# Kernel optimization log

Hardware: AMD Instinct MI355X
Metric: run time of the kernel (lower is better)

Reference implementation:

```python
import jax, jax.numpy as jnp
import numpy as np

B, N, C, F = 8, 3, 64, 128
H = W = 128


def _up2(x):
    # nearest-neighbor upsample by 2 on the last two axes
    return jnp.repeat(jnp.repeat(x, 2, axis=-2), 2, axis=-1)


def setup_inputs() -> dict:
    key = jax.random.key(0)
    ks = jax.random.split(key, 12)
    s = lambda k, shp, fan: jax.random.normal(k, shp, jnp.float32) * (1.0 / np.sqrt(fan))
    return {
        "contexts": jax.random.normal(ks[0], (B, N, C, H, W), jnp.float32),
        "mainstream": jax.random.normal(ks[1], (B, F, H // 2, W // 2), jnp.float32),
        "Wc": s(ks[2], (C, C), C),        # W_context 1x1 conv weight [out,in]
        "bc": jnp.zeros((C,), jnp.float32),
        "Wf": s(ks[3], (C, F), F),        # W_feat 1x1
        "bf": jnp.zeros((C,), jnp.float32),
        "Wk": s(ks[4], (C, F), F),        # W_key_feat 1x1
        "bk": jnp.zeros((C,), jnp.float32),
        "Vw": s(ks[5], (C, F, 3, 3), F * 9),  # values_conv 3x3, OIHW
        "Vb": jnp.zeros((C,), jnp.float32),
    }


def reference(contexts, mainstream, Wc, bc, Wf, bf, Wk, bk, Vw, Vb):
    # contexts: [B,N,C,H,W], mainstream: [B,F,h,w]
    bias = lambda b: b[None, :, None, None]
    queries = jnp.einsum('bfhw,cf->bchw', mainstream, Wf) + bias(bf)       # [B,C,h,w]
    keys_m = jnp.einsum('bfhw,cf->bchw', mainstream, Wk) + bias(bk)        # [B,C,h,w]
    values = jax.lax.conv_general_dilated(
        mainstream, Vw, (1, 1), 'SAME',
        dimension_numbers=('NCHW', 'OIHW', 'NCHW')) + bias(Vb)             # [B,C,h,w]

    # stack contexts with upsampled mainstream keys, project with W_context (1x1)
    keys_stack = jnp.concatenate([contexts, _up2(keys_m)[:, None]], axis=1)  # [B,N+1,C,H,W]
    keys_proj = jnp.einsum('bnchw,dc->bndhw', keys_stack, Wc) + bc[None, None, :, None, None]

    q_up = _up2(queries)                                                    # [B,C,H,W]
    logits = jnp.einsum('bnchw,bchw->bnhw', keys_proj, q_up)                # [B,N+1,H,W]
    attn = jax.nn.softmax(logits, axis=1)                                   # softmax over contexts

    vals_stack = jnp.concatenate([contexts, _up2(values)[:, None]], axis=1) # [B,N+1,C,H,W]
    out = jnp.einsum('bnchw,bnhw->bchw', vals_stack, attn)                  # [B,C,H,W]
    return out
```

## Files before the change

kernel.cpp:

```cpp
#include <hip/hip_runtime.h>
#include <math.h>

#define CH   64
#define FD   128
#define HS   64
#define FS   128
#define NB   8
#define NCTX 3

#define WS_BQ   4227072
#define WS_AVH  4227136
#define WS_AQH  4264000
#define WS_AQL  4268096
#define WS_AKH  4272192
#define WS_AKL  4276288

typedef short  s16x8  __attribute__((ext_vector_type(8)));
typedef float  f32x16 __attribute__((ext_vector_type(16)));

__device__ inline unsigned short bf16_rne(float x) {
  unsigned u = __float_as_uint(x);
  u += 0x7FFFu + ((u >> 16) & 1u);
  return (unsigned short)(u >> 16);
}
__device__ inline void split2(float x, unsigned short& h, unsigned short& l) {
  h = bf16_rne(x);
  l = bf16_rne(x - __uint_as_float((unsigned)h << 16));
}

__global__ __launch_bounds__(256) void afrag_prep(
    const float* __restrict__ Wc, const float* __restrict__ Wf,
    const float* __restrict__ bf, const float* __restrict__ Wk,
    const float* __restrict__ Vw, float* __restrict__ ws) {
  int id = blockIdx.x * 256 + threadIdx.x;
  unsigned short* avh = (unsigned short*)(ws + WS_AVH);
  unsigned short* aqh = (unsigned short*)(ws + WS_AQH);
  unsigned short* aql = (unsigned short*)(ws + WS_AQL);
  unsigned short* akh = (unsigned short*)(ws + WS_AKH);
  unsigned short* akl = (unsigned short*)(ws + WS_AKL);

  if (id < 9216) {
    int tile = id / 4608, rem = id % 4608;
    int q = rem >> 6, l = rem & 63;
    int am = l & 31, kh = l >> 5;
    int c = tile * 32 + am, tap = q >> 3, kf = q & 7;
#pragma unroll
    for (int j = 0; j < 8; ++j) {
      int f = kf * 16 + kh * 8 + j;
      avh[id * 8 + j] = bf16_rne(Vw[(c * FD + f) * 9 + tap]);
    }
  } else if (id < 10240) {
    int i2 = id - 9216;
    int tile = i2 >> 9, rem = i2 & 511;
    int q = rem >> 6, l = rem & 63;
    int am = l & 31, kh = l >> 5;
    int c = tile * 32 + am;
#pragma unroll
    for (int j = 0; j < 8; ++j) {
      int f = q * 16 + kh * 8 + j;
      float acc = 0.f;
      for (int d = 0; d < CH; ++d)
        acc = fmaf(Wc[d * CH + c], Wf[d * FD + f], acc);
      unsigned short h, lo; split2(acc, h, lo);
      aqh[i2 * 8 + j] = h; aql[i2 * 8 + j] = lo;
    }
  } else if (id < 11264) {
    int i3 = id - 10240;
    int tile = i3 >> 9, rem = i3 & 511;
    int q = rem >> 6, l = rem & 63;
    int am = l & 31, kh = l >> 5;
    int c = tile * 32 + am;
#pragma unroll
    for (int j = 0; j < 8; ++j) {
      int f = q * 16 + kh * 8 + j;
      unsigned short h, lo; split2(Wk[c * FD + f], h, lo);
      akh[i3 * 8 + j] = h; akl[i3 * 8 + j] = lo;
    }
  } else if (id < 11328) {
    int c = id - 11264;
    float acc = 0.f;
    for (int d = 0; d < CH; ++d) acc = fmaf(Wc[d * CH + c], bf[d], acc);
    ws[WS_BQ + c] = acc;
  }
}

__global__ __launch_bounds__(512) void fused_kernel(
    const float* __restrict__ m, const float* __restrict__ Vb,
    const float* __restrict__ bk, const float* __restrict__ ctx,
    float* __restrict__ out, const float* __restrict__ ws) {
  const int b = blockIdx.x >> 6, y = blockIdx.x & 63;
  const int t = threadIdx.x, lane = t & 63;
  const int wave = __builtin_amdgcn_readfirstlane(t >> 6);
  const int am = lane & 31, kh = lane >> 5;

  __shared__ __align__(16) union {
    short HI[3][8][66][2][8];
    struct {
      float  QT[CH * HS];
      float  VAL[CH * HS];
      float4 wpart[2][4][3][16];
      float  L3row[HS];
    } p;
  } U;
  __shared__ float l3red[2][64];

  if (t < 96) {
    int row = t / 32, kf = (t >> 2) & 7, khh = (t >> 1) & 1, col = (t & 1) * 65;
    s16x8 z;
#pragma unroll
    for (int j = 0; j < 8; ++j) z[j] = 0;
    *(s16x8*)&U.HI[row][kf][col][khh][0] = z;
  }

#pragma unroll
  for (int i = 0; i < 6; ++i) {
    const int tk = wave * 6 + i;
    const int row = tk >> 4, kf = (tk >> 1) & 7, khh = tk & 1;
    const int yy = y + row - 1;
    s16x8 hi;
    if (yy >= 0 && yy < HS) {
#pragma unroll
      for (int j = 0; j < 8; ++j) {
        const int f = kf * 16 + khh * 8 + j;
        hi[j] = (short)bf16_rne(m[((b * FD + f) * HS + yy) * HS + lane]);
      }
    } else {
#pragma unroll
      for (int j = 0; j < 8; ++j) hi[j] = 0;
    }
    *(s16x8*)&U.HI[row][kf][lane + 1][khh][0] = hi;
  }
  __syncthreads();

  const int ct = (wave >> 1) & 1;
  const int xh = wave & 1;
  const int x0 = xh * 32, ch0 = ct * 32;

  f32x16 acc, q1, q2, k1, k2;
  float l3part = 0.f;

  if (wave < 4) {
    const unsigned short* avh = (const unsigned short*)(ws + WS_AVH);
#pragma unroll
    for (int i = 0; i < 16; ++i) acc[i] = 0.f;
#pragma unroll 8
    for (int q = 0; q < 72; ++q) {
      const int tap = q >> 3, kf = q & 7;
      const s16x8 ah = *(const s16x8*)(avh + ((ct * 72 + q) * 64 + lane) * 8);
      const s16x8 bh = *(const s16x8*)&U.HI[tap / 3][kf][x0 + am + tap % 3][kh][0];
      acc = __builtin_amdgcn_mfma_f32_32x32x16_bf16(ah, bh, acc, 0, 0, 0);
    }
  } else {
    const unsigned short* aqh = (const unsigned short*)(ws + WS_AQH);
    const unsigned short* aql = (const unsigned short*)(ws + WS_AQL);
    const unsigned short* akh = (const unsigned short*)(ws + WS_AKH);
    const unsigned short* akl = (const unsigned short*)(ws + WS_AKL);
#pragma unroll
    for (int i = 0; i < 16; ++i) { q1[i] = 0.f; q2[i] = 0.f; k1[i] = 0.f; k2[i] = 0.f; }
#pragma unroll
    for (int q = 0; q < 8; ++q) {
      const s16x8 bh = *(const s16x8*)&U.HI[1][q][x0 + am + 1][kh][0];
      s16x8 bl;
#pragma unroll
      for (int j = 0; j < 8; ++j) {
        const float mv = m[((b * FD + q * 16 + kh * 8 + j) * HS + y) * HS + x0 + am];
        const float hf = __uint_as_float(((unsigned)(unsigned short)bh[j]) << 16);
        bl[j] = (short)bf16_rne(mv - hf);
      }
      const s16x8 ah = *(const s16x8*)(aqh + ((ct * 8 + q) * 64 + lane) * 8);
      const s16x8 al = *(const s16x8*)(aql + ((ct * 8 + q) * 64 + lane) * 8);
      const s16x8 kah = *(const s16x8*)(akh + ((ct * 8 + q) * 64 + lane) * 8);
      const s16x8 kal = *(const s16x8*)(akl + ((ct * 8 + q) * 64 + lane) * 8);
      q1 = __builtin_amdgcn_mfma_f32_32x32x16_bf16(ah, bh, q1, 0, 0, 0);
      q1 = __builtin_amdgcn_mfma_f32_32x32x16_bf16(al, bh, q1, 0, 0, 0);
      q2 = __builtin_amdgcn_mfma_f32_32x32x16_bf16(ah, bl, q2, 0, 0, 0);
      k1 = __builtin_amdgcn_mfma_f32_32x32x16_bf16(kah, bh, k1, 0, 0, 0);
      k1 = __builtin_amdgcn_mfma_f32_32x32x16_bf16(kal, bh, k1, 0, 0, 0);
      k2 = __builtin_amdgcn_mfma_f32_32x32x16_bf16(kah, bl, k2, 0, 0, 0);
    }
  }
  __syncthreads();

  if (wave < 4) {
#pragma unroll
    for (int r = 0; r < 16; ++r) {
      const int c = ch0 + (r & 3) + 8 * (r >> 2) + 4 * kh;
      U.p.VAL[c * HS + x0 + am] = acc[r] + Vb[c];
    }
  } else {
#pragma unroll
    for (int r = 0; r < 16; ++r) {
      const int c = ch0 + (r & 3) + 8 * (r >> 2) + 4 * kh;
      const float qvv = q1[r] + q2[r] + ws[WS_BQ + c];
      const float kvv = k1[r] + k2[r] + bk[c];
      U.p.QT[c * HS + x0 + am] = qvv;
      l3part = fmaf(qvv, kvv, l3part);
    }
    if (ct == 1) l3red[xh][lane] = l3part;
  }
  __syncthreads();

  if (wave == 4 || wave == 5) {
    float s = l3part + l3red[xh][lane];
    s += __shfl_xor(s, 32, 64);
    if (kh == 0) U.p.L3row[x0 + am] = s;
  }
  __syncthreads();

  const int u    = t >> 8;
  const int tt   = t & 255;
  const int quad = tt & 15;
  const int cg   = tt >> 4;
  const int wv   = tt >> 6;
  const int c0   = cg * 4;
  const int hrow = 2 * y + u;
  const int cs = FS * FS, ns = CH * FS * FS;

  float* op = out + (size_t)(b * CH) * FS * FS + (size_t)hrow * FS;
  const float* cb = ctx + (size_t)(b * NCTX * CH) * cs + (size_t)hrow * FS;

#pragma unroll 1
  for (int x2 = 0; x2 < 2; ++x2) {
    const int x = x2 * 64 + quad * 4;
    const int w2 = x >> 1;

    float4 cv[3][4];
    float2 qv[4];
#pragma unroll
    for (int j = 0; j < 4; ++j) {
      const int c = c0 + j;
      cv[0][j] = *(const float4*)(cb + x + c * cs);
      cv[1][j] = *(const float4*)(cb + x + ns + c * cs);
      cv[2][j] = *(const float4*)(cb + x + 2 * ns + c * cs);
      qv[j] = *(const float2*)&U.p.QT[c * HS + w2];
    }

    float4 pl[3];
#pragma unroll
    for (int n = 0; n < 3; ++n) {
      pl[n].x = pl[n].y = pl[n].z = pl[n].w = 0.f;
#pragma unroll
      for (int j = 0; j < 4; ++j) {
        pl[n].x = fmaf(cv[n][j].x, qv[j].x, pl[n].x);
        pl[n].y = fmaf(cv[n][j].y, qv[j].x, pl[n].y);
        pl[n].z = fmaf(cv[n][j].z, qv[j].y, pl[n].z);
        pl[n].w = fmaf(cv[n][j].w, qv[j].y, pl[n].w);
      }
    }

#pragma unroll
    for (int n = 0; n < 3; ++n) {
      pl[n].x += __shfl_xor(pl[n].x, 16, 64);
      pl[n].y += __shfl_xor(pl[n].y, 16, 64);
      pl[n].z += __shfl_xor(pl[n].z, 16, 64);
      pl[n].w += __shfl_xor(pl[n].w, 16, 64);
      pl[n].x += __shfl_xor(pl[n].x, 32, 64);
      pl[n].y += __shfl_xor(pl[n].y, 32, 64);
      pl[n].z += __shfl_xor(pl[n].z, 32, 64);
      pl[n].w += __shfl_xor(pl[n].w, 32, 64);
    }
    __syncthreads();
    if ((lane >> 4) == 0) {
#pragma unroll
      for (int n = 0; n < 3; ++n) U.p.wpart[u][wv][n][quad] = pl[n];
    }
    __syncthreads();

    float4 L[3];
#pragma unroll
    for (int n = 0; n < 3; ++n) {
      const float4 p0 = U.p.wpart[u][0][n][quad];
      const float4 p1 = U.p.wpart[u][1][n][quad];
      const float4 p2 = U.p.wpart[u][2][n][quad];
      const float4 p3 = U.p.wpart[u][3][n][quad];
      L[n].x = (p0.x + p1.x) + (p2.x + p3.x);
      L[n].y = (p0.y + p1.y) + (p2.y + p3.y);
      L[n].z = (p0.z + p1.z) + (p2.z + p3.z);
      L[n].w = (p0.w + p1.w) + (p2.w + p3.w);
    }
    const float2 l3v = *(const float2*)&U.p.L3row[w2];

    float A0[4], A1[4], A2[4], A3[4];
    const float* L0p = (const float*)&L[0];
    const float* L1p = (const float*)&L[1];
    const float* L2p = (const float*)&L[2];
#pragma unroll
    for (int k = 0; k < 4; ++k) {
      float L0 = L0p[k], L1 = L1p[k], L2 = L2p[k];
      float L3 = (k < 2) ? l3v.x : l3v.y;
      float mx = fmaxf(fmaxf(L0, L1), fmaxf(L2, L3));
      float e0 = __expf(L0 - mx), e1 = __expf(L1 - mx);
      float e2 = __expf(L2 - mx), e3 = __expf(L3 - mx);
      float inv = 1.f / (e0 + e1 + e2 + e3);
      A0[k] = e0 * inv; A1[k] = e1 * inv; A2[k] = e2 * inv; A3[k] = e3 * inv;
    }

#pragma unroll
    for (int j = 0; j < 4; ++j) {
      const int c = c0 + j;
      const float2 vv = *(const float2*)&U.p.VAL[c * HS + w2];
      float4 o;
      o.x = fmaf(A0[0], cv[0][j].x, fmaf(A1[0], cv[1][j].x, fmaf(A2[0], cv[2][j].x, A3[0] * vv.x)));
      o.y = fmaf(A0[1], cv[0][j].y, fmaf(A1[1], cv[1][j].y, fmaf(A2[1], cv[2][j].y, A3[1] * vv.x)));
      o.z = fmaf(A0[2], cv[0][j].z, fmaf(A1[2], cv[1][j].z, fmaf(A2[2], cv[2][j].z, A3[2] * vv.y)));
      o.w = fmaf(A0[3], cv[0][j].w, fmaf(A1[3], cv[1][j].w, fmaf(A2[3], cv[2][j].w, A3[3] * vv.y)));
      *(float4*)(op + x + c * cs) = o;
    }
  }
}

extern "C" void kernel_launch(void* const* d_in, const int* in_sizes, int n_in,
                              void* d_out, int out_size, void* d_ws, size_t ws_size,
                              hipStream_t stream) {
  const float* ctx = (const float*)d_in[0];
  const float* ms  = (const float*)d_in[1];
  const float* Wc  = (const float*)d_in[2];
  const float* Wf  = (const float*)d_in[4];
  const float* bf  = (const float*)d_in[5];
  const float* Wk  = (const float*)d_in[6];
  const float* bk  = (const float*)d_in[7];
  const float* Vw  = (const float*)d_in[8];
  const float* Vb  = (const float*)d_in[9];
  float* ws  = (float*)d_ws;
  float* out = (float*)d_out;

  afrag_prep<<<45, 256, 0, stream>>>(Wc, Wf, bf, Wk, Vw, ws);
  fused_kernel<<<NB * HS, 512, 0, stream>>>(ms, Vb, bk, ctx, out, ws);
}
```

Baseline: 244.9 us.

## Precompute bf16 low parts in LDS and software-pipeline MFMA weight loads

During the staging phase, the bf16 residual (low part) of the center mainstream row is computed once and stored in a new LDS array. This replaces the per-wave global reloads and conversions that the Q/K waves did inside their MFMA loop. Both MFMA loops are restructured to double-buffer their weight-fragment loads from the workspace, prefetching the next group while the current one runs through MFMA. Launch bounds now request 4 blocks per CU. That adds register pressure from the prefetch buffers and a little extra LDS.

```diff
diff --git a/kernel.cpp b/kernel.cpp
--- a/kernel.cpp
+++ b/kernel.cpp
@@ -84,7 +84,7 @@
   }
 }
 
-__global__ __launch_bounds__(512) void fused_kernel(
+__global__ __launch_bounds__(512, 4) void fused_kernel(
     const float* __restrict__ m, const float* __restrict__ Vb,
     const float* __restrict__ bk, const float* __restrict__ ctx,
     float* __restrict__ out, const float* __restrict__ ws) {
@@ -102,6 +102,7 @@
       float  L3row[HS];
     } p;
   } U;
+  __shared__ __align__(16) short BL[8][66][2][8];
   __shared__ float l3red[2][64];
 
   if (t < 96) {
@@ -119,10 +120,22 @@
     const int yy = y + row - 1;
     s16x8 hi;
     if (yy >= 0 && yy < HS) {
+      float mv[8];
 #pragma unroll
       for (int j = 0; j < 8; ++j) {
         const int f = kf * 16 + khh * 8 + j;
-        hi[j] = (short)bf16_rne(m[((b * FD + f) * HS + yy) * HS + lane]);
+        mv[j] = m[((b * FD + f) * HS + yy) * HS + lane];
+      }
+#pragma unroll
+      for (int j = 0; j < 8; ++j) hi[j] = (short)bf16_rne(mv[j]);
+      if (row == 1) {
+        s16x8 lo;
+#pragma unroll
+        for (int j = 0; j < 8; ++j) {
+          const float hf = __uint_as_float(((unsigned)(unsigned short)hi[j]) << 16);
+          lo[j] = (short)bf16_rne(mv[j] - hf);
+        }
+        *(s16x8*)&BL[kf][lane + 1][khh][0] = lo;
       }
     } else {
 #pragma unroll
@@ -143,12 +156,25 @@
     const unsigned short* avh = (const unsigned short*)(ws + WS_AVH);
 #pragma unroll
     for (int i = 0; i < 16; ++i) acc[i] = 0.f;
-#pragma unroll 8
-    for (int q = 0; q < 72; ++q) {
-      const int tap = q >> 3, kf = q & 7;
-      const s16x8 ah = *(const s16x8*)(avh + ((ct * 72 + q) * 64 + lane) * 8);
-      const s16x8 bh = *(const s16x8*)&U.HI[tap / 3][kf][x0 + am + tap % 3][kh][0];
-      acc = __builtin_amdgcn_mfma_f32_32x32x16_bf16(ah, bh, acc, 0, 0, 0);
+    s16x8 A[8];
+#pragma unroll
+    for (int i = 0; i < 8; ++i)
+      A[i] = *(const s16x8*)(avh + ((ct * 72 + i) * 64 + lane) * 8);
+#pragma unroll 1
+    for (int g = 0; g < 9; ++g) {
+      s16x8 Bv[8];
+      const int qb = (g < 8) ? (g * 8 + 8) : 0;
+#pragma unroll
+      for (int i = 0; i < 8; ++i)
+        Bv[i] = *(const s16x8*)(avh + ((ct * 72 + qb + i) * 64 + lane) * 8);
+      const int tap = g, tr = tap / 3, tc = tap % 3;
+#pragma unroll
+      for (int i = 0; i < 8; ++i) {
+        const s16x8 bh = *(const s16x8*)&U.HI[tr][i][x0 + am + tc][kh][0];
+        acc = __builtin_amdgcn_mfma_f32_32x32x16_bf16(A[i], bh, acc, 0, 0, 0);
+      }
+#pragma unroll
+      for (int i = 0; i < 8; ++i) A[i] = Bv[i];
     }
   } else {
     const unsigned short* aqh = (const unsigned short*)(ws + WS_AQH);
@@ -157,26 +183,26 @@
     const unsigned short* akl = (const unsigned short*)(ws + WS_AKL);
 #pragma unroll
     for (int i = 0; i < 16; ++i) { q1[i] = 0.f; q2[i] = 0.f; k1[i] = 0.f; k2[i] = 0.f; }
-#pragma unroll
+    s16x8 ah  = *(const s16x8*)(aqh + ((ct * 8 + 0) * 64 + lane) * 8);
+    s16x8 al  = *(const s16x8*)(aql + ((ct * 8 + 0) * 64 + lane) * 8);
+    s16x8 kah = *(const s16x8*)(akh + ((ct * 8 + 0) * 64 + lane) * 8);
+    s16x8 kal = *(const s16x8*)(akl + ((ct * 8 + 0) * 64 + lane) * 8);
+#pragma unroll 1
     for (int q = 0; q < 8; ++q) {
+      const int qn = (q < 7) ? (q + 1) : 0;
+      s16x8 ahn  = *(const s16x8*)(aqh + ((ct * 8 + qn) * 64 + lane) * 8);
+      s16x8 aln  = *(const s16x8*)(aql + ((ct * 8 + qn) * 64 + lane) * 8);
+      s16x8 kahn = *(const s16x8*)(akh + ((ct * 8 + qn) * 64 + lane) * 8);
+      s16x8 kaln = *(const s16x8*)(akl + ((ct * 8 + qn) * 64 + lane) * 8);
       const s16x8 bh = *(const s16x8*)&U.HI[1][q][x0 + am + 1][kh][0];
-      s16x8 bl;
-#pragma unroll
-      for (int j = 0; j < 8; ++j) {
-        const float mv = m[((b * FD + q * 16 + kh * 8 + j) * HS + y) * HS + x0 + am];
-        const float hf = __uint_as_float(((unsigned)(unsigned short)bh[j]) << 16);
-        bl[j] = (short)bf16_rne(mv - hf);
-      }
-      const s16x8 ah = *(const s16x8*)(aqh + ((ct * 8 + q) * 64 + lane) * 8);
-      const s16x8 al = *(const s16x8*)(aql + ((ct * 8 + q) * 64 + lane) * 8);
-      const s16x8 kah = *(const s16x8*)(akh + ((ct * 8 + q) * 64 + lane) * 8);
-      const s16x8 kal = *(const s16x8*)(akl + ((ct * 8 + q) * 64 + lane) * 8);
-      q1 = __builtin_amdgcn_mfma_f32_32x32x16_bf16(ah, bh, q1, 0, 0, 0);
-      q1 = __builtin_amdgcn_mfma_f32_32x32x16_bf16(al, bh, q1, 0, 0, 0);
-      q2 = __builtin_amdgcn_mfma_f32_32x32x16_bf16(ah, bl, q2, 0, 0, 0);
+      const s16x8 bl = *(const s16x8*)&BL[q][x0 + am + 1][kh][0];
+      q1 = __builtin_amdgcn_mfma_f32_32x32x16_bf16(ah,  bh, q1, 0, 0, 0);
+      q1 = __builtin_amdgcn_mfma_f32_32x32x16_bf16(al,  bh, q1, 0, 0, 0);
+      q2 = __builtin_amdgcn_mfma_f32_32x32x16_bf16(ah,  bl, q2, 0, 0, 0);
       k1 = __builtin_amdgcn_mfma_f32_32x32x16_bf16(kah, bh, k1, 0, 0, 0);
       k1 = __builtin_amdgcn_mfma_f32_32x32x16_bf16(kal, bh, k1, 0, 0, 0);
       k2 = __builtin_amdgcn_mfma_f32_32x32x16_bf16(kah, bl, k2, 0, 0, 0);
+      ah = ahn; al = aln; kah = kahn; kal = kaln;
     }
   }
   __syncthreads();
```

After: 249.0 us. No clear change (+1.7%).
